# Kernel optimization log

Hardware: AMD Instinct MI355X
Metric: run time of the kernel (lower is better)

Reference implementation:

```python
import jax, jax.numpy as jnp
import numpy as np

B, T, D, H, E = 4, 2048, 1024, 2048, 8
TOP_K = int(E * 0.25)  # = 2


def setup_inputs() -> dict:
    key = jax.random.key(0)
    ks = jax.random.split(key, 6)
    x = jax.random.normal(ks[0], (B, T, D), dtype=jnp.float32)
    gate = jax.random.normal(ks[1], (D, E), dtype=jnp.float32)
    # per-expert 2-layer MLP params (D -> H -> D), stacked over experts
    W1 = jax.random.normal(ks[2], (E, D, H), dtype=jnp.float32) * (D ** -0.5)
    b1 = jnp.zeros((E, H), dtype=jnp.float32)
    W2 = jax.random.normal(ks[3], (E, H, D), dtype=jnp.float32) * (H ** -0.5)
    b2 = jnp.zeros((E, D), dtype=jnp.float32)
    return {"x": x, "gate": gate, "W1": W1, "b1": b1, "W2": W2, "b2": b2}


def reference(x, gate, W1, b1, W2, b2):
    # gating: softmax over experts, then top-k mask, renormalize (L1 over experts)
    raw_gate = jax.nn.softmax(jnp.einsum('btd,de->bte', x, gate), axis=-1)  # [B,T,E]
    topk_scores, topk_idx = jax.lax.top_k(raw_gate, TOP_K)                   # [B,T,k]
    mask = jax.nn.one_hot(topk_idx, E, dtype=raw_gate.dtype).sum(axis=-2)    # [B,T,E]
    gate_topk = mask * raw_gate
    gate_topk = gate_topk / jnp.maximum(gate_topk.sum(axis=-1, keepdims=True), 1e-12)
    # dense all-expert compute (faithful to the original: every expert sees every token)
    h = jax.nn.relu(jnp.einsum('btd,edh->beth', x, W1) + b1[None, :, None, :])  # [B,E,T,H]
    expert_out = jnp.einsum('beth,ehd->betd', h, W2) + b2[None, :, None, :]     # [B,E,T,D]
    # weighted combine
    out = jnp.einsum('bte,betd->btd', gate_topk, expert_out)  # [B,T,D]
    return out
```

## Files before the change

### kernel.cpp

```cpp
#include <hip/hip_runtime.h>

#define E_      8
#define D_      1024
#define H_      2048
#define TOKENS  8192
#define RROWS   16384
#define HPAD_ROWS (RROWS + 256)

using bf16x8 = __attribute__((ext_vector_type(8))) __bf16;
using f32x4  = __attribute__((ext_vector_type(4))) float;

__device__ __forceinline__ unsigned short f2bf(float f) {
  unsigned u = __builtin_bit_cast(unsigned, f);
  u += 0x7fffu + ((u >> 16) & 1u);
  return (unsigned short)(u >> 16);
}
__device__ __forceinline__ float bf2f(unsigned short u) {
  unsigned v = (unsigned)u << 16;
  return __builtin_bit_cast(float, v);
}

#define GLDS16(g, l) __builtin_amdgcn_global_load_lds( \
    (const __attribute__((address_space(1))) unsigned int*)(g), \
    (__attribute__((address_space(3))) unsigned int*)(l), 16, 0, 0)

#define SBAR() asm volatile("s_barrier" ::: "memory")


__global__ void transpose_cvt_kernel(const float* __restrict__ src,
                                     unsigned short* __restrict__ dst,
                                     int R, int C) {
  int tilesC = C >> 6, tilesR = R >> 6;
  int per = tilesR * tilesC;
  int b = blockIdx.x;
  int e = b / per, rem = b % per;
  int rb = rem / tilesC, cb = rem % tilesC;
  __shared__ float tile[64][65];
  const float* s = src + (size_t)e * R * C;
  unsigned short* d = dst + (size_t)e * R * C;
  int r0 = rb << 6, c0 = cb << 6;
#pragma unroll
  for (int i = 0; i < 16; i++) {
    int idx = threadIdx.x + i * 256;
    int lr = idx >> 6, lc = idx & 63;
    tile[lr][lc] = s[(size_t)(r0 + lr) * C + (c0 + lc)];
  }
  __syncthreads();
#pragma unroll
  for (int i = 0; i < 16; i++) {
    int idx = threadIdx.x + i * 256;
    int lr = idx >> 6, lc = idx & 63;
    d[(size_t)(c0 + lr) * R + (r0 + lc)] = f2bf(tile[lc][lr]);
  }
}

__global__ void gating_kernel(const float* __restrict__ x, const float* __restrict__ gate,
                              unsigned short* __restrict__ xb,
                              int* __restrict__ sel, float* __restrict__ wsel) {
  int lane = threadIdx.x & 63, wid = threadIdx.x >> 6;
  int t = (blockIdx.x << 2) + wid;
  const float* xr = x + (size_t)t * D_;
  unsigned short* xbr = xb + (size_t)t * D_;
  float acc[8];
#pragma unroll
  for (int e = 0; e < 8; e++) acc[e] = 0.f;
#pragma unroll
  for (int i = 0; i < 4; i++) {
    int d0 = (i << 8) + (lane << 2);
    float4 xv = *reinterpret_cast<const float4*>(xr + d0);
    ushort4 o = make_ushort4(f2bf(xv.x), f2bf(xv.y), f2bf(xv.z), f2bf(xv.w));
    *reinterpret_cast<ushort4*>(xbr + d0) = o;
    float xa[4] = {xv.x, xv.y, xv.z, xv.w};
#pragma unroll
    for (int j = 0; j < 4; j++) {
      const float4* g4 = reinterpret_cast<const float4*>(gate + (size_t)(d0 + j) * 8);
      float4 ga = g4[0], gb = g4[1];
      acc[0] += xa[j] * ga.x; acc[1] += xa[j] * ga.y;
      acc[2] += xa[j] * ga.z; acc[3] += xa[j] * ga.w;
      acc[4] += xa[j] * gb.x; acc[5] += xa[j] * gb.y;
      acc[6] += xa[j] * gb.z; acc[7] += xa[j] * gb.w;
    }
  }
#pragma unroll
  for (int e = 0; e < 8; e++) {
#pragma unroll
    for (int off = 32; off; off >>= 1) acc[e] += __shfl_xor(acc[e], off);
  }
  if (lane == 0) {
    int i0 = 0; float v0 = acc[0];
#pragma unroll
    for (int e = 1; e < 8; e++) if (acc[e] > v0) { v0 = acc[e]; i0 = e; }
    int i1 = -1; float v1 = -3.4e38f;
#pragma unroll
    for (int e = 0; e < 8; e++) if (e != i0 && acc[e] > v1) { v1 = acc[e]; i1 = e; }
    float p1 = expf(v1 - v0);
    float inv = 1.f / (1.f + p1);
    sel[t * 2] = i0; sel[t * 2 + 1] = i1;
    wsel[t * 2] = inv; wsel[t * 2 + 1] = p1 * inv;
  }
}

__global__ __launch_bounds__(1024) void route_kernel(
    const int* __restrict__ sel, int* __restrict__ cnt, int* __restrict__ off,
    int* __restrict__ tok_id, int* __restrict__ pos) {
  const int tid = threadIdx.x;
  const int lane = tid & 63, wid = tid >> 6;
  __shared__ int wtot[16][8];
  __shared__ int woff[16][8];
  __shared__ int offs[8];
  int sv[16];
  const int s0 = tid << 4;
#pragma unroll
  for (int q = 0; q < 4; q++) {
    int4 v = reinterpret_cast<const int4*>(sel + s0)[q];
    sv[q * 4 + 0] = v.x; sv[q * 4 + 1] = v.y;
    sv[q * 4 + 2] = v.z; sv[q * 4 + 3] = v.w;
  }
  int h[8];
#pragma unroll
  for (int e = 0; e < 8; e++) h[e] = 0;
#pragma unroll
  for (int j = 0; j < 16; j++) {
    int ev = sv[j];
#pragma unroll
    for (int e = 0; e < 8; e++) h[e] += (ev == e) ? 1 : 0;
  }
  int excl[8];
#pragma unroll
  for (int e = 0; e < 8; e++) {
    int v = h[e];
#pragma unroll
    for (int d = 1; d < 64; d <<= 1) {
      int u = __shfl_up(v, d);
      if (lane >= d) v += u;
    }
    excl[e] = v - h[e];
    if (lane == 63) wtot[wid][e] = v;
  }
  __syncthreads();
  if (tid == 0) {
    int run[8];
#pragma unroll
    for (int e = 0; e < 8; e++) run[e] = 0;
    for (int w = 0; w < 16; w++)
#pragma unroll
      for (int e = 0; e < 8; e++) { woff[w][e] = run[e]; run[e] += wtot[w][e]; }
    int a = 0;
    for (int e = 0; e < 8; e++) { offs[e] = a; off[e] = a; cnt[e] = run[e]; a += run[e]; }
  }
  __syncthreads();
  int base[8];
#pragma unroll
  for (int e = 0; e < 8; e++) base[e] = offs[e] + woff[wid][e] + excl[e];
#pragma unroll
  for (int j = 0; j < 16; j++) {
    int ev = sv[j];
    int p = 0;
#pragma unroll
    for (int e = 0; e < 8; e++) if (ev == e) { p = base[e]; base[e] = p + 1; }
    pos[s0 + j] = p;
    tok_id[p] = (s0 + j) >> 1;
  }
}


#define STAGE256(slot, kh) do { \
  const size_t ko = (size_t)(kh) << 7; \
  _Pragma("unroll") \
  for (int i = 0; i < 4; i++) { \
    GLDS16(Ab + aO[i] + ko, (char*)&Asm[slot][0] + (i << 13) + (wid << 10)); \
    GLDS16(Bb + bO[i] + ko, (char*)&Bsm[slot][0] + (i << 13) + (wid << 10)); \
  } \
} while (0)

__global__ __launch_bounds__(512, 2) void gemm1_kernel(
    const unsigned short* __restrict__ xb,
    const unsigned short* __restrict__ w1t,
    const float* __restrict__ b1,
    unsigned short* __restrict__ hbuf,
    const int* __restrict__ tok_id,
    const int* __restrict__ cnt, const int* __restrict__ off) {
  const int nwg = E_ * 64 * 8;
  const int raw = blockIdx.x;
  const int bid = (raw & 7) * (nwg >> 3) + (raw >> 3);
  const int e  = bid >> 9;
  const int rb = (bid >> 3) & 63;
  const int cb = bid & 7;
  const int rows = cnt[e];
  const int m0 = rb << 8;
  if (m0 >= rows) return;
  const int base = off[e];
  const int tid = threadIdx.x, lane = tid & 63, wid = tid >> 6;
  const int wr = wid >> 2, wc = wid & 3;

  __shared__ __align__(16) unsigned short Asm[2][256 * 64];
  __shared__ __align__(16) unsigned short Bsm[2][256 * 64];

  const size_t swz = (size_t)(((tid & 7) ^ ((tid >> 3) & 7)) << 4);
  const int srow = tid >> 3;
  const int n0 = cb << 8;
  size_t aO[4], bO[4];
  const char* Ab = (const char*)xb;
  const char* Bb = (const char*)w1t + (size_t)e * H_ * D_ * 2;
#pragma unroll
  for (int i = 0; i < 4; i++) {
    int r = (i << 6) + srow;
    int ar = m0 + r; if (ar >= rows) ar = rows - 1;
    aO[i] = (size_t)tok_id[base + ar] * (D_ * 2) + swz;
    bO[i] = (size_t)(n0 + r) * (D_ * 2) + swz;
  }

  const int aRow = ((wr << 7) + (lane & 15)) * 128;
  const int bRow = ((wc << 6) + (lane & 15)) * 128;
  const int cby0 = (((lane >> 4)) ^ (lane & 7)) << 4;
  const int cby1 = ((4 + (lane >> 4)) ^ (lane & 7)) << 4;

  f32x4 acc[8][4] = {};
  const int KH = D_ / 64;

  STAGE256(0, 0);
  STAGE256(1, 1);
  asm volatile("s_waitcnt vmcnt(8)" ::: "memory");
  SBAR();

  for (int kh = 0; kh < KH; ++kh) {
    const int cur = kh & 1;
    const char* Ap = (const char*)&Asm[cur][0] + aRow;
    const char* Bp = (const char*)&Bsm[cur][0] + bRow;
    bf16x8 a[8], b[4];
#pragma unroll
    for (int m = 0; m < 8; m++) a[m] = *(const bf16x8*)(Ap + cby0 + m * 2048);
#pragma unroll
    for (int n = 0; n < 4; n++) b[n] = *(const bf16x8*)(Bp + cby0 + n * 2048);
    __builtin_amdgcn_s_setprio(1);
#pragma unroll
    for (int m = 0; m < 8; m++)
#pragma unroll
      for (int n = 0; n < 4; n++)
        acc[m][n] = __builtin_amdgcn_mfma_f32_16x16x32_bf16(a[m], b[n], acc[m][n], 0, 0, 0);
    __builtin_amdgcn_s_setprio(0);
#pragma unroll
    for (int m = 0; m < 8; m++) a[m] = *(const bf16x8*)(Ap + cby1 + m * 2048);
#pragma unroll
    for (int n = 0; n < 4; n++) b[n] = *(const bf16x8*)(Bp + cby1 + n * 2048);
    asm volatile("s_waitcnt lgkmcnt(0)" ::: "memory");
    __builtin_amdgcn_sched_barrier(0);
    SBAR();
    if (kh + 2 < KH) STAGE256(cur, kh + 2);
    __builtin_amdgcn_s_setprio(1);
#pragma unroll
    for (int m = 0; m < 8; m++)
#pragma unroll
      for (int n = 0; n < 4; n++)
        acc[m][n] = __builtin_amdgcn_mfma_f32_16x16x32_bf16(a[m], b[n], acc[m][n], 0, 0, 0);
    __builtin_amdgcn_s_setprio(0);
    if (kh + 2 < KH) {
      asm volatile("s_waitcnt vmcnt(8)" ::: "memory");
    } else if (kh + 1 < KH) {
      asm volatile("s_waitcnt vmcnt(0)" ::: "memory");
    }
    SBAR();
  }

  const int rcnt = rows - m0;
  const float* b1e = b1 + e * H_;
#pragma unroll
  for (int m = 0; m < 8; m++) {
#pragma unroll
    for (int q = 0; q < 4; q++) {
      int rl = (wr << 7) + (m << 4) + ((lane >> 4) << 2) + q;
      if (rl < rcnt) {
        unsigned short* hrow = hbuf + (size_t)(base + m0 + rl) * H_;
#pragma unroll
        for (int n = 0; n < 4; n++) {
          int ncol = n0 + (wc << 6) + (n << 4) + (lane & 15);
          float v = acc[m][n][q] + b1e[ncol];
          hrow[ncol] = f2bf(fmaxf(v, 0.f));
        }
      }
    }
  }
}

__global__ __launch_bounds__(512, 2) void gemm2_kernel(
    const unsigned short* __restrict__ hbuf,
    const unsigned short* __restrict__ w2t,
    unsigned short* __restrict__ eout,
    const int* __restrict__ cnt, const int* __restrict__ off) {
  const int nwg = E_ * 64 * 4;
  const int raw = blockIdx.x;
  const int bid = (raw & 7) * (nwg >> 3) + (raw >> 3);
  const int e  = bid >> 8;
  const int rb = (bid >> 2) & 63;
  const int cb = bid & 3;
  const int rows = cnt[e];
  const int m0 = rb << 8;
  if (m0 >= rows) return;
  const int base = off[e];
  const int tid = threadIdx.x, lane = tid & 63, wid = tid >> 6;
  const int wr = wid >> 2, wc = wid & 3;

  __shared__ __align__(16) unsigned short Asm[2][256 * 64];
  __shared__ __align__(16) unsigned short Bsm[2][256 * 64];

  const size_t swz = (size_t)(((tid & 7) ^ ((tid >> 3) & 7)) << 4);
  const int srow = tid >> 3;
  const int n0 = cb << 8;
  size_t aO[4], bO[4];
  const char* Ab = (const char*)hbuf;
  const char* Bb = (const char*)w2t + (size_t)e * D_ * H_ * 2;
#pragma unroll
  for (int i = 0; i < 4; i++) {
    int r = (i << 6) + srow;
    aO[i] = (size_t)(base + m0 + r) * (H_ * 2) + swz;
    bO[i] = (size_t)(n0 + r) * (H_ * 2) + swz;
  }

  const int aRow = ((wr << 7) + (lane & 15)) * 128;
  const int bRow = ((wc << 6) + (lane & 15)) * 128;
  const int cby0 = (((lane >> 4)) ^ (lane & 7)) << 4;
  const int cby1 = ((4 + (lane >> 4)) ^ (lane & 7)) << 4;

  f32x4 acc[8][4] = {};
  const int KH = H_ / 64;

  STAGE256(0, 0);
  STAGE256(1, 1);
  asm volatile("s_waitcnt vmcnt(8)" ::: "memory");
  SBAR();

  for (int kh = 0; kh < KH; ++kh) {
    const int cur = kh & 1;
    const char* Ap = (const char*)&Asm[cur][0] + aRow;
    const char* Bp = (const char*)&Bsm[cur][0] + bRow;
    bf16x8 a[8], b[4];
#pragma unroll
    for (int m = 0; m < 8; m++) a[m] = *(const bf16x8*)(Ap + cby0 + m * 2048);
#pragma unroll
    for (int n = 0; n < 4; n++) b[n] = *(const bf16x8*)(Bp + cby0 + n * 2048);
    __builtin_amdgcn_s_setprio(1);
#pragma unroll
    for (int m = 0; m < 8; m++)
#pragma unroll
      for (int n = 0; n < 4; n++)
        acc[m][n] = __builtin_amdgcn_mfma_f32_16x16x32_bf16(a[m], b[n], acc[m][n], 0, 0, 0);
    __builtin_amdgcn_s_setprio(0);
#pragma unroll
    for (int m = 0; m < 8; m++) a[m] = *(const bf16x8*)(Ap + cby1 + m * 2048);
#pragma unroll
    for (int n = 0; n < 4; n++) b[n] = *(const bf16x8*)(Bp + cby1 + n * 2048);
    asm volatile("s_waitcnt lgkmcnt(0)" ::: "memory");
    __builtin_amdgcn_sched_barrier(0);
    SBAR();
    if (kh + 2 < KH) STAGE256(cur, kh + 2);
    __builtin_amdgcn_s_setprio(1);
#pragma unroll
    for (int m = 0; m < 8; m++)
#pragma unroll
      for (int n = 0; n < 4; n++)
        acc[m][n] = __builtin_amdgcn_mfma_f32_16x16x32_bf16(a[m], b[n], acc[m][n], 0, 0, 0);
    __builtin_amdgcn_s_setprio(0);
    if (kh + 2 < KH) {
      asm volatile("s_waitcnt vmcnt(8)" ::: "memory");
    } else if (kh + 1 < KH) {
      asm volatile("s_waitcnt vmcnt(0)" ::: "memory");
    }
    SBAR();
  }

  const int rcnt = rows - m0;
#pragma unroll
  for (int m = 0; m < 8; m++) {
#pragma unroll
    for (int q = 0; q < 4; q++) {
      int rl = (wr << 7) + (m << 4) + ((lane >> 4) << 2) + q;
      if (rl < rcnt) {
        unsigned short* erow = eout + (size_t)(base + m0 + rl) * D_;
#pragma unroll
        for (int n = 0; n < 4; n++) {
          int ncol = n0 + (wc << 6) + (n << 4) + (lane & 15);
          erow[ncol] = f2bf(acc[m][n][q]);
        }
      }
    }
  }
}

__global__ void combine_kernel(const unsigned short* __restrict__ eout,
                               const float* __restrict__ b2,
                               const int* __restrict__ sel, const float* __restrict__ wsel,
                               const int* __restrict__ pos,
                               float* __restrict__ out) {
  int t = blockIdx.x;
  int d = threadIdx.x << 2;
  int e0 = sel[t * 2], e1 = sel[t * 2 + 1];
  float w0 = wsel[t * 2], w1 = wsel[t * 2 + 1];
  int p0 = pos[t * 2], p1 = pos[t * 2 + 1];
  ushort4 y0 = *reinterpret_cast<const ushort4*>(eout + (size_t)p0 * D_ + d);
  ushort4 y1 = *reinterpret_cast<const ushort4*>(eout + (size_t)p1 * D_ + d);
  float4 c0 = *reinterpret_cast<const float4*>(b2 + (size_t)e0 * D_ + d);
  float4 c1 = *reinterpret_cast<const float4*>(b2 + (size_t)e1 * D_ + d);
  float4 o;
  o.x = w0 * (bf2f(y0.x) + c0.x) + w1 * (bf2f(y1.x) + c1.x);
  o.y = w0 * (bf2f(y0.y) + c0.y) + w1 * (bf2f(y1.y) + c1.y);
  o.z = w0 * (bf2f(y0.z) + c0.z) + w1 * (bf2f(y1.z) + c1.z);
  o.w = w0 * (bf2f(y0.w) + c0.w) + w1 * (bf2f(y1.w) + c1.w);
  *reinterpret_cast<float4*>(out + (size_t)t * D_ + d) = o;
}


extern "C" void kernel_launch(void* const* d_in, const int* in_sizes, int n_in,
                              void* d_out, int out_size, void* d_ws, size_t ws_size,
                              hipStream_t stream) {
  (void)in_sizes; (void)n_in; (void)ws_size; (void)out_size;
  const float* x    = (const float*)d_in[0];
  const float* gate = (const float*)d_in[1];
  const float* W1   = (const float*)d_in[2];
  const float* b1   = (const float*)d_in[3];
  const float* W2   = (const float*)d_in[4];
  const float* b2   = (const float*)d_in[5];
  float* out = (float*)d_out;

  char* p = (char*)d_ws;
  unsigned short* xb   = (unsigned short*)p; p += (size_t)TOKENS * D_ * 2;
  unsigned short* w1t  = (unsigned short*)p; p += (size_t)E_ * H_ * D_ * 2;
  unsigned short* w2t  = (unsigned short*)p; p += (size_t)E_ * D_ * H_ * 2;
  unsigned short* hbuf = (unsigned short*)p; p += (size_t)HPAD_ROWS * H_ * 2;
  int*   tok  = (int*)p;   p += (size_t)RROWS * 4;
  int*   pos  = (int*)p;   p += (size_t)TOKENS * 2 * 4;
  int*   sel  = (int*)p;   p += (size_t)TOKENS * 2 * 4;
  float* wsel = (float*)p; p += (size_t)TOKENS * 2 * 4;
  int* cnt    = (int*)p;   p += 32 * 4;
  int* off    = (int*)p;   p += 32 * 4;
  unsigned short* eout = w1t;

  transpose_cvt_kernel<<<E_ * (D_ / 64) * (H_ / 64), 256, 0, stream>>>(W1, w1t, D_, H_);
  transpose_cvt_kernel<<<E_ * (H_ / 64) * (D_ / 64), 256, 0, stream>>>(W2, w2t, H_, D_);
  gating_kernel<<<TOKENS / 4, 256, 0, stream>>>(x, gate, xb, sel, wsel);
  route_kernel<<<1, 1024, 0, stream>>>(sel, cnt, off, tok, pos);
  gemm1_kernel<<<E_ * 64 * 8, 512, 0, stream>>>(xb, w1t, b1, hbuf, tok, cnt, off);
  gemm2_kernel<<<E_ * 64 * 4, 512, 0, stream>>>(hbuf, w2t, eout, cnt, off);
  combine_kernel<<<TOKENS, 256, 0, stream>>>(eout, b2, sel, wsel, pos, out);
}
```

Measured before the change: 327.6 us.

## Fuse prologue kernels, retile grouped GEMMs to 128x256 with triple-buffered LDS

Merges the two weight transpose/convert kernels and the gating kernel into one launch. Both expert GEMMs move from 256x256 tiles with 512 threads and double buffering to 128x256 tiles with 256 threads and a 3-stage LDS ring. Staging loads are interleaved between the two MFMA halves, and the mid-iteration barrier plus lgkmcnt wait are dropped. The combine kernel now handles four tokens per block, one wave per token. The smaller M tile cuts padding waste on uneven expert counts but raises B-operand reloads, and one block per CU (launch_bounds 256,1) may reduce latency hiding.

```diff
diff --git a/kernel.cpp b/kernel.cpp
--- a/kernel.cpp
+++ b/kernel.cpp
@@ -5,7 +5,7 @@
 #define H_      2048
 #define TOKENS  8192
 #define RROWS   16384
-#define HPAD_ROWS (RROWS + 256)
+#define HPAD_ROWS (RROWS + 128)
 
 using bf16x8 = __attribute__((ext_vector_type(8))) __bf16;
 using f32x4  = __attribute__((ext_vector_type(4))) float;
@@ -27,15 +27,67 @@
 #define SBAR() asm volatile("s_barrier" ::: "memory")
 
 
-__global__ void transpose_cvt_kernel(const float* __restrict__ src,
-                                     unsigned short* __restrict__ dst,
-                                     int R, int C) {
-  int tilesC = C >> 6, tilesR = R >> 6;
-  int per = tilesR * tilesC;
+__global__ void prologue_kernel(const float* __restrict__ x, const float* __restrict__ gate,
+                                unsigned short* __restrict__ xb,
+                                int* __restrict__ sel, float* __restrict__ wsel,
+                                const float* __restrict__ W1, unsigned short* __restrict__ w1t,
+                                const float* __restrict__ W2, unsigned short* __restrict__ w2t) {
+  __shared__ float tile[64][65];
   int b = blockIdx.x;
+  const int NG = TOKENS / 4;
+  if (b < NG) {
+    int lane = threadIdx.x & 63, wid = threadIdx.x >> 6;
+    int t = (b << 2) + wid;
+    const float* xr = x + (size_t)t * D_;
+    unsigned short* xbr = xb + (size_t)t * D_;
+    float acc[8];
+#pragma unroll
+    for (int e = 0; e < 8; e++) acc[e] = 0.f;
+#pragma unroll
+    for (int i = 0; i < 4; i++) {
+      int d0 = (i << 8) + (lane << 2);
+      float4 xv = *reinterpret_cast<const float4*>(xr + d0);
+      ushort4 o = make_ushort4(f2bf(xv.x), f2bf(xv.y), f2bf(xv.z), f2bf(xv.w));
+      *reinterpret_cast<ushort4*>(xbr + d0) = o;
+      float xa[4] = {xv.x, xv.y, xv.z, xv.w};
+#pragma unroll
+      for (int j = 0; j < 4; j++) {
+        const float4* g4 = reinterpret_cast<const float4*>(gate + (size_t)(d0 + j) * 8);
+        float4 ga = g4[0], gb = g4[1];
+        acc[0] += xa[j] * ga.x; acc[1] += xa[j] * ga.y;
+        acc[2] += xa[j] * ga.z; acc[3] += xa[j] * ga.w;
+        acc[4] += xa[j] * gb.x; acc[5] += xa[j] * gb.y;
+        acc[6] += xa[j] * gb.z; acc[7] += xa[j] * gb.w;
+      }
+    }
+#pragma unroll
+    for (int e = 0; e < 8; e++) {
+#pragma unroll
+      for (int off = 32; off; off >>= 1) acc[e] += __shfl_xor(acc[e], off);
+    }
+    if (lane == 0) {
+      int i0 = 0; float v0 = acc[0];
+#pragma unroll
+      for (int e = 1; e < 8; e++) if (acc[e] > v0) { v0 = acc[e]; i0 = e; }
+      int i1 = -1; float v1 = -3.4e38f;
+#pragma unroll
+      for (int e = 0; e < 8; e++) if (e != i0 && acc[e] > v1) { v1 = acc[e]; i1 = e; }
+      float p1 = expf(v1 - v0);
+      float inv = 1.f / (1.f + p1);
+      sel[t * 2] = i0; sel[t * 2 + 1] = i1;
+      wsel[t * 2] = inv; wsel[t * 2 + 1] = p1 * inv;
+    }
+    return;
+  }
+  b -= NG;
+  const int nb1 = E_ * (D_ >> 6) * (H_ >> 6);
+  const float* src; unsigned short* dst; int R, C;
+  if (b < nb1) { src = W1; dst = w1t; R = D_; C = H_; }
+  else         { src = W2; dst = w2t; R = H_; C = D_; b -= nb1; }
+  int tilesC = C >> 6;
+  int per = (R >> 6) * tilesC;
   int e = b / per, rem = b % per;
   int rb = rem / tilesC, cb = rem % tilesC;
-  __shared__ float tile[64][65];
   const float* s = src + (size_t)e * R * C;
   unsigned short* d = dst + (size_t)e * R * C;
   int r0 = rb << 6, c0 = cb << 6;
@@ -51,52 +103,6 @@
     int idx = threadIdx.x + i * 256;
     int lr = idx >> 6, lc = idx & 63;
     d[(size_t)(c0 + lr) * R + (r0 + lc)] = f2bf(tile[lc][lr]);
-  }
-}
-
-__global__ void gating_kernel(const float* __restrict__ x, const float* __restrict__ gate,
-                              unsigned short* __restrict__ xb,
-                              int* __restrict__ sel, float* __restrict__ wsel) {
-  int lane = threadIdx.x & 63, wid = threadIdx.x >> 6;
-  int t = (blockIdx.x << 2) + wid;
-  const float* xr = x + (size_t)t * D_;
-  unsigned short* xbr = xb + (size_t)t * D_;
-  float acc[8];
-#pragma unroll
-  for (int e = 0; e < 8; e++) acc[e] = 0.f;
-#pragma unroll
-  for (int i = 0; i < 4; i++) {
-    int d0 = (i << 8) + (lane << 2);
-    float4 xv = *reinterpret_cast<const float4*>(xr + d0);
-    ushort4 o = make_ushort4(f2bf(xv.x), f2bf(xv.y), f2bf(xv.z), f2bf(xv.w));
-    *reinterpret_cast<ushort4*>(xbr + d0) = o;
-    float xa[4] = {xv.x, xv.y, xv.z, xv.w};
-#pragma unroll
-    for (int j = 0; j < 4; j++) {
-      const float4* g4 = reinterpret_cast<const float4*>(gate + (size_t)(d0 + j) * 8);
-      float4 ga = g4[0], gb = g4[1];
-      acc[0] += xa[j] * ga.x; acc[1] += xa[j] * ga.y;
-      acc[2] += xa[j] * ga.z; acc[3] += xa[j] * ga.w;
-      acc[4] += xa[j] * gb.x; acc[5] += xa[j] * gb.y;
-      acc[6] += xa[j] * gb.z; acc[7] += xa[j] * gb.w;
-    }
-  }
-#pragma unroll
-  for (int e = 0; e < 8; e++) {
-#pragma unroll
-    for (int off = 32; off; off >>= 1) acc[e] += __shfl_xor(acc[e], off);
-  }
-  if (lane == 0) {
-    int i0 = 0; float v0 = acc[0];
-#pragma unroll
-    for (int e = 1; e < 8; e++) if (acc[e] > v0) { v0 = acc[e]; i0 = e; }
-    int i1 = -1; float v1 = -3.4e38f;
-#pragma unroll
-    for (int e = 0; e < 8; e++) if (e != i0 && acc[e] > v1) { v1 = acc[e]; i1 = e; }
-    float p1 = expf(v1 - v0);
-    float inv = 1.f / (1.f + p1);
-    sel[t * 2] = i0; sel[t * 2 + 1] = i1;
-    wsel[t * 2] = inv; wsel[t * 2 + 1] = p1 * inv;
   }
 }
 
@@ -164,16 +170,7 @@
 }
 
 
-#define STAGE256(slot, kh) do { \
-  const size_t ko = (size_t)(kh) << 7; \
-  _Pragma("unroll") \
-  for (int i = 0; i < 4; i++) { \
-    GLDS16(Ab + aO[i] + ko, (char*)&Asm[slot][0] + (i << 13) + (wid << 10)); \
-    GLDS16(Bb + bO[i] + ko, (char*)&Bsm[slot][0] + (i << 13) + (wid << 10)); \
-  } \
-} while (0)
-
-__global__ __launch_bounds__(512, 2) void gemm1_kernel(
+__global__ __launch_bounds__(256, 1) void gemm1_kernel(
     const unsigned short* __restrict__ xb,
     const unsigned short* __restrict__ w1t,
     const float* __restrict__ b1,
@@ -187,51 +184,58 @@
   const int rb = (bid >> 3) & 63;
   const int cb = bid & 7;
   const int rows = cnt[e];
-  const int m0 = rb << 8;
+  const int m0 = rb << 7;
   if (m0 >= rows) return;
   const int base = off[e];
   const int tid = threadIdx.x, lane = tid & 63, wid = tid >> 6;
-  const int wr = wid >> 2, wc = wid & 3;
-
-  __shared__ __align__(16) unsigned short Asm[2][256 * 64];
-  __shared__ __align__(16) unsigned short Bsm[2][256 * 64];
-
-  const size_t swz = (size_t)(((tid & 7) ^ ((tid >> 3) & 7)) << 4);
-  const int srow = tid >> 3;
+  const int wc = wid;
+
+  __shared__ __align__(16) unsigned short Asm[3][128 * 64];
+  __shared__ __align__(16) unsigned short Bsm[3][256 * 64];
+
+  const unsigned swz = ((lane & 7) ^ (lane >> 3)) << 4;
   const int n0 = cb << 8;
-  size_t aO[4], bO[4];
+  unsigned gA[4];
+#pragma unroll
+  for (int i = 0; i < 4; i++) {
+    int r = ((wid << 2) + i) * 8 + (lane >> 3);
+    int ar = m0 + r; if (ar >= rows) ar = rows - 1;
+    gA[i] = (unsigned)tok_id[base + ar] * (D_ * 2) + swz;
+  }
+  const unsigned gB0 = (unsigned)(n0 + (wid << 6) + (lane >> 3)) * (D_ * 2) + swz;
   const char* Ab = (const char*)xb;
   const char* Bb = (const char*)w1t + (size_t)e * H_ * D_ * 2;
-#pragma unroll
-  for (int i = 0; i < 4; i++) {
-    int r = (i << 6) + srow;
-    int ar = m0 + r; if (ar >= rows) ar = rows - 1;
-    aO[i] = (size_t)tok_id[base + ar] * (D_ * 2) + swz;
-    bO[i] = (size_t)(n0 + r) * (D_ * 2) + swz;
-  }
-
-  const int aRow = ((wr << 7) + (lane & 15)) * 128;
-  const int bRow = ((wc << 6) + (lane & 15)) * 128;
+
+#define G1_STAGE_A(s, t) do { const size_t ko = (size_t)(t) << 7; \
+  _Pragma("unroll") for (int i = 0; i < 4; i++) \
+    GLDS16(Ab + gA[i] + ko, &Asm[s][((wid << 2) + i) << 9]); } while (0)
+#define G1_STAGE_B(s, t) do { const size_t ko = (size_t)(t) << 7; \
+  _Pragma("unroll") for (int i = 0; i < 8; i++) \
+    GLDS16(Bb + gB0 + i * 16384 + ko, &Bsm[s][((wid << 3) + i) << 9]); } while (0)
+
+  const int aRd = (lane & 15) * 128;
+  const int bRd = ((wc << 6) + (lane & 15)) * 128;
   const int cby0 = (((lane >> 4)) ^ (lane & 7)) << 4;
   const int cby1 = ((4 + (lane >> 4)) ^ (lane & 7)) << 4;
 
   f32x4 acc[8][4] = {};
-  const int KH = D_ / 64;
-
-  STAGE256(0, 0);
-  STAGE256(1, 1);
-  asm volatile("s_waitcnt vmcnt(8)" ::: "memory");
+  const int KT = D_ / 64;
+
+  G1_STAGE_A(0, 0); G1_STAGE_B(0, 0);
+  G1_STAGE_A(1, 1); G1_STAGE_B(1, 1);
+  asm volatile("s_waitcnt vmcnt(12)" ::: "memory");
   SBAR();
 
-  for (int kh = 0; kh < KH; ++kh) {
-    const int cur = kh & 1;
-    const char* Ap = (const char*)&Asm[cur][0] + aRow;
-    const char* Bp = (const char*)&Bsm[cur][0] + bRow;
+  int sl = 0, ss = 2;
+  for (int t = 0; t < KT; ++t) {
+    const char* Ap = (const char*)&Asm[sl][0] + aRd;
+    const char* Bp = (const char*)&Bsm[sl][0] + bRd;
     bf16x8 a[8], b[4];
 #pragma unroll
+    for (int n = 0; n < 4; n++) b[n] = *(const bf16x8*)(Bp + cby0 + n * 2048);
+#pragma unroll
     for (int m = 0; m < 8; m++) a[m] = *(const bf16x8*)(Ap + cby0 + m * 2048);
-#pragma unroll
-    for (int n = 0; n < 4; n++) b[n] = *(const bf16x8*)(Bp + cby0 + n * 2048);
+    if (t + 2 < KT) G1_STAGE_A(ss, t + 2);
     __builtin_amdgcn_s_setprio(1);
 #pragma unroll
     for (int m = 0; m < 8; m++)
@@ -240,13 +244,10 @@
         acc[m][n] = __builtin_amdgcn_mfma_f32_16x16x32_bf16(a[m], b[n], acc[m][n], 0, 0, 0);
     __builtin_amdgcn_s_setprio(0);
 #pragma unroll
+    for (int n = 0; n < 4; n++) b[n] = *(const bf16x8*)(Bp + cby1 + n * 2048);
+#pragma unroll
     for (int m = 0; m < 8; m++) a[m] = *(const bf16x8*)(Ap + cby1 + m * 2048);
-#pragma unroll
-    for (int n = 0; n < 4; n++) b[n] = *(const bf16x8*)(Bp + cby1 + n * 2048);
-    asm volatile("s_waitcnt lgkmcnt(0)" ::: "memory");
-    __builtin_amdgcn_sched_barrier(0);
-    SBAR();
-    if (kh + 2 < KH) STAGE256(cur, kh + 2);
+    if (t + 2 < KT) G1_STAGE_B(ss, t + 2);
     __builtin_amdgcn_s_setprio(1);
 #pragma unroll
     for (int m = 0; m < 8; m++)
@@ -254,12 +255,14 @@
       for (int n = 0; n < 4; n++)
         acc[m][n] = __builtin_amdgcn_mfma_f32_16x16x32_bf16(a[m], b[n], acc[m][n], 0, 0, 0);
     __builtin_amdgcn_s_setprio(0);
-    if (kh + 2 < KH) {
-      asm volatile("s_waitcnt vmcnt(8)" ::: "memory");
-    } else if (kh + 1 < KH) {
+    if (t + 2 < KT) {
+      asm volatile("s_waitcnt vmcnt(12)" ::: "memory");
+    } else if (t + 1 < KT) {
       asm volatile("s_waitcnt vmcnt(0)" ::: "memory");
     }
     SBAR();
+    sl = (sl == 2) ? 0 : sl + 1;
+    ss = (ss == 2) ? 0 : ss + 1;
   }
 
   const int rcnt = rows - m0;
@@ -268,7 +271,7 @@
   for (int m = 0; m < 8; m++) {
 #pragma unroll
     for (int q = 0; q < 4; q++) {
-      int rl = (wr << 7) + (m << 4) + ((lane >> 4) << 2) + q;
+      int rl = (m << 4) + ((lane >> 4) << 2) + q;
       if (rl < rcnt) {
         unsigned short* hrow = hbuf + (size_t)(base + m0 + rl) * H_;
 #pragma unroll
@@ -282,7 +285,7 @@
   }
 }
 
-__global__ __launch_bounds__(512, 2) void gemm2_kernel(
+__global__ __launch_bounds__(256, 1) void gemm2_kernel(
     const unsigned short* __restrict__ hbuf,
     const unsigned short* __restrict__ w2t,
     unsigned short* __restrict__ eout,
@@ -294,50 +297,52 @@
   const int rb = (bid >> 2) & 63;
   const int cb = bid & 3;
   const int rows = cnt[e];
-  const int m0 = rb << 8;
+  const int m0 = rb << 7;
   if (m0 >= rows) return;
   const int base = off[e];
   const int tid = threadIdx.x, lane = tid & 63, wid = tid >> 6;
-  const int wr = wid >> 2, wc = wid & 3;
-
-  __shared__ __align__(16) unsigned short Asm[2][256 * 64];
-  __shared__ __align__(16) unsigned short Bsm[2][256 * 64];
-
-  const size_t swz = (size_t)(((tid & 7) ^ ((tid >> 3) & 7)) << 4);
-  const int srow = tid >> 3;
+  const int wc = wid;
+
+  __shared__ __align__(16) unsigned short Asm[3][128 * 64];
+  __shared__ __align__(16) unsigned short Bsm[3][256 * 64];
+
+  const unsigned swz = ((lane & 7) ^ (lane >> 3)) << 4;
   const int n0 = cb << 8;
-  size_t aO[4], bO[4];
+  const unsigned gA0 = (unsigned)(base + m0 + (wid << 5) + (lane >> 3)) * (H_ * 2) + swz;
+  const unsigned gB0 = (unsigned)(n0 + (wid << 6) + (lane >> 3)) * (H_ * 2) + swz;
   const char* Ab = (const char*)hbuf;
   const char* Bb = (const char*)w2t + (size_t)e * D_ * H_ * 2;
-#pragma unroll
-  for (int i = 0; i < 4; i++) {
-    int r = (i << 6) + srow;
-    aO[i] = (size_t)(base + m0 + r) * (H_ * 2) + swz;
-    bO[i] = (size_t)(n0 + r) * (H_ * 2) + swz;
-  }
-
-  const int aRow = ((wr << 7) + (lane & 15)) * 128;
-  const int bRow = ((wc << 6) + (lane & 15)) * 128;
+
+#define G2_STAGE_A(s, t) do { const size_t ko = (size_t)(t) << 7; \
+  _Pragma("unroll") for (int i = 0; i < 4; i++) \
+    GLDS16(Ab + gA0 + i * 32768 + ko, &Asm[s][((wid << 2) + i) << 9]); } while (0)
+#define G2_STAGE_B(s, t) do { const size_t ko = (size_t)(t) << 7; \
+  _Pragma("unroll") for (int i = 0; i < 8; i++) \
+    GLDS16(Bb + gB0 + i * 32768 + ko, &Bsm[s][((wid << 3) + i) << 9]); } while (0)
+
+  const int aRd = (lane & 15) * 128;
+  const int bRd = ((wc << 6) + (lane & 15)) * 128;
   const int cby0 = (((lane >> 4)) ^ (lane & 7)) << 4;
   const int cby1 = ((4 + (lane >> 4)) ^ (lane & 7)) << 4;
 
   f32x4 acc[8][4] = {};
-  const int KH = H_ / 64;
-
-  STAGE256(0, 0);
-  STAGE256(1, 1);
-  asm volatile("s_waitcnt vmcnt(8)" ::: "memory");
+  const int KT = H_ / 64;
+
+  G2_STAGE_A(0, 0); G2_STAGE_B(0, 0);
+  G2_STAGE_A(1, 1); G2_STAGE_B(1, 1);
+  asm volatile("s_waitcnt vmcnt(12)" ::: "memory");
   SBAR();
 
-  for (int kh = 0; kh < KH; ++kh) {
-    const int cur = kh & 1;
-    const char* Ap = (const char*)&Asm[cur][0] + aRow;
-    const char* Bp = (const char*)&Bsm[cur][0] + bRow;
+  int sl = 0, ss = 2;
+  for (int t = 0; t < KT; ++t) {
+    const char* Ap = (const char*)&Asm[sl][0] + aRd;
+    const char* Bp = (const char*)&Bsm[sl][0] + bRd;
     bf16x8 a[8], b[4];
 #pragma unroll
+    for (int n = 0; n < 4; n++) b[n] = *(const bf16x8*)(Bp + cby0 + n * 2048);
+#pragma unroll
     for (int m = 0; m < 8; m++) a[m] = *(const bf16x8*)(Ap + cby0 + m * 2048);
-#pragma unroll
-    for (int n = 0; n < 4; n++) b[n] = *(const bf16x8*)(Bp + cby0 + n * 2048);
+    if (t + 2 < KT) G2_STAGE_A(ss, t + 2);
     __builtin_amdgcn_s_setprio(1);
 #pragma unroll
     for (int m = 0; m < 8; m++)
@@ -346,13 +351,10 @@
         acc[m][n] = __builtin_amdgcn_mfma_f32_16x16x32_bf16(a[m], b[n], acc[m][n], 0, 0, 0);
     __builtin_amdgcn_s_setprio(0);
 #pragma unroll
+    for (int n = 0; n < 4; n++) b[n] = *(const bf16x8*)(Bp + cby1 + n * 2048);
+#pragma unroll
     for (int m = 0; m < 8; m++) a[m] = *(const bf16x8*)(Ap + cby1 + m * 2048);
-#pragma unroll
-    for (int n = 0; n < 4; n++) b[n] = *(const bf16x8*)(Bp + cby1 + n * 2048);
-    asm volatile("s_waitcnt lgkmcnt(0)" ::: "memory");
-    __builtin_amdgcn_sched_barrier(0);
-    SBAR();
-    if (kh + 2 < KH) STAGE256(cur, kh + 2);
+    if (t + 2 < KT) G2_STAGE_B(ss, t + 2);
     __builtin_amdgcn_s_setprio(1);
 #pragma unroll
     for (int m = 0; m < 8; m++)
@@ -360,12 +362,14 @@
       for (int n = 0; n < 4; n++)
         acc[m][n] = __builtin_amdgcn_mfma_f32_16x16x32_bf16(a[m], b[n], acc[m][n], 0, 0, 0);
     __builtin_amdgcn_s_setprio(0);
-    if (kh + 2 < KH) {
-      asm volatile("s_waitcnt vmcnt(8)" ::: "memory");
-    } else if (kh + 1 < KH) {
+    if (t + 2 < KT) {
+      asm volatile("s_waitcnt vmcnt(12)" ::: "memory");
+    } else if (t + 1 < KT) {
       asm volatile("s_waitcnt vmcnt(0)" ::: "memory");
     }
     SBAR();
+    sl = (sl == 2) ? 0 : sl + 1;
+    ss = (ss == 2) ? 0 : ss + 1;
   }
 
   const int rcnt = rows - m0;
@@ -373,7 +377,7 @@
   for (int m = 0; m < 8; m++) {
 #pragma unroll
     for (int q = 0; q < 4; q++) {
-      int rl = (wr << 7) + (m << 4) + ((lane >> 4) << 2) + q;
+      int rl = (m << 4) + ((lane >> 4) << 2) + q;
       if (rl < rcnt) {
         unsigned short* erow = eout + (size_t)(base + m0 + rl) * D_;
 #pragma unroll
@@ -391,21 +395,30 @@
                                const int* __restrict__ sel, const float* __restrict__ wsel,
                                const int* __restrict__ pos,
                                float* __restrict__ out) {
-  int t = blockIdx.x;
-  int d = threadIdx.x << 2;
+  int t = (blockIdx.x << 2) + (threadIdx.x >> 6);
+  int lane = threadIdx.x & 63;
   int e0 = sel[t * 2], e1 = sel[t * 2 + 1];
   float w0 = wsel[t * 2], w1 = wsel[t * 2 + 1];
   int p0 = pos[t * 2], p1 = pos[t * 2 + 1];
-  ushort4 y0 = *reinterpret_cast<const ushort4*>(eout + (size_t)p0 * D_ + d);
-  ushort4 y1 = *reinterpret_cast<const ushort4*>(eout + (size_t)p1 * D_ + d);
-  float4 c0 = *reinterpret_cast<const float4*>(b2 + (size_t)e0 * D_ + d);
-  float4 c1 = *reinterpret_cast<const float4*>(b2 + (size_t)e1 * D_ + d);
-  float4 o;
-  o.x = w0 * (bf2f(y0.x) + c0.x) + w1 * (bf2f(y1.x) + c1.x);
-  o.y = w0 * (bf2f(y0.y) + c0.y) + w1 * (bf2f(y1.y) + c1.y);
-  o.z = w0 * (bf2f(y0.z) + c0.z) + w1 * (bf2f(y1.z) + c1.z);
-  o.w = w0 * (bf2f(y0.w) + c0.w) + w1 * (bf2f(y1.w) + c1.w);
-  *reinterpret_cast<float4*>(out + (size_t)t * D_ + d) = o;
+  const unsigned short* y0r = eout + (size_t)p0 * D_;
+  const unsigned short* y1r = eout + (size_t)p1 * D_;
+  const float* c0r = b2 + (size_t)e0 * D_;
+  const float* c1r = b2 + (size_t)e1 * D_;
+  float* orow = out + (size_t)t * D_;
+#pragma unroll
+  for (int j = 0; j < 4; j++) {
+    int d = (j << 8) + (lane << 2);
+    ushort4 y0 = *reinterpret_cast<const ushort4*>(y0r + d);
+    ushort4 y1 = *reinterpret_cast<const ushort4*>(y1r + d);
+    float4 c0 = *reinterpret_cast<const float4*>(c0r + d);
+    float4 c1 = *reinterpret_cast<const float4*>(c1r + d);
+    float4 o;
+    o.x = w0 * (bf2f(y0.x) + c0.x) + w1 * (bf2f(y1.x) + c1.x);
+    o.y = w0 * (bf2f(y0.y) + c0.y) + w1 * (bf2f(y1.y) + c1.y);
+    o.z = w0 * (bf2f(y0.z) + c0.z) + w1 * (bf2f(y1.z) + c1.z);
+    o.w = w0 * (bf2f(y0.w) + c0.w) + w1 * (bf2f(y1.w) + c1.w);
+    *reinterpret_cast<float4*>(orow + d) = o;
+  }
 }
 
 
@@ -434,11 +447,12 @@
   int* off    = (int*)p;   p += 32 * 4;
   unsigned short* eout = w1t;
 
-  transpose_cvt_kernel<<<E_ * (D_ / 64) * (H_ / 64), 256, 0, stream>>>(W1, w1t, D_, H_);
-  transpose_cvt_kernel<<<E_ * (H_ / 64) * (D_ / 64), 256, 0, stream>>>(W2, w2t, H_, D_);
-  gating_kernel<<<TOKENS / 4, 256, 0, stream>>>(x, gate, xb, sel, wsel);
+  const int nb1 = E_ * (D_ / 64) * (H_ / 64);
+  const int nb2 = E_ * (H_ / 64) * (D_ / 64);
+  prologue_kernel<<<TOKENS / 4 + nb1 + nb2, 256, 0, stream>>>(
+      x, gate, xb, sel, wsel, W1, w1t, W2, w2t);
   route_kernel<<<1, 1024, 0, stream>>>(sel, cnt, off, tok, pos);
-  gemm1_kernel<<<E_ * 64 * 8, 512, 0, stream>>>(xb, w1t, b1, hbuf, tok, cnt, off);
-  gemm2_kernel<<<E_ * 64 * 4, 512, 0, stream>>>(hbuf, w2t, eout, cnt, off);
-  combine_kernel<<<TOKENS, 256, 0, stream>>>(eout, b2, sel, wsel, pos, out);
-}
+  gemm1_kernel<<<E_ * 64 * 8, 256, 0, stream>>>(xb, w1t, b1, hbuf, tok, cnt, off);
+  gemm2_kernel<<<E_ * 64 * 4, 256, 0, stream>>>(hbuf, w2t, eout, cnt, off);
+  combine_kernel<<<TOKENS / 4, 256, 0, stream>>>(eout, b2, sel, wsel, pos, out);
+}
```

Result: slower. 419.4 us (+28.0%).
